# Optimization experiments

Hardware: AMD Instinct MI355X
Metric: run time of the kernel (lower is better)

Reference implementation:

```python
import jax, jax.numpy as jnp
import numpy as np
from jax import lax

B, S, M, D, H, T = 8, 128, 128, 256, 256, 256  # M == S required by reshape_adj; D == H required by tag FFNs and edge h0


def setup_inputs() -> dict:
    key = jax.random.key(0)
    ks = jax.random.split(key, 26)
    w = lambda k, shape: (jax.random.normal(k, shape, jnp.float32) * 0.05)
    lengths = jax.random.randint(ks[0], (B,), S // 2, S + 1)
    mask = (jnp.arange(S)[None, :] < lengths[:, None]).astype(jnp.int32)
    return {
        "input": jax.random.normal(ks[1], (B, S, D), jnp.float32),
        "tag_embeddings": jax.random.normal(ks[2], (B, S, 128), jnp.float32),
        "mask": mask,
        "head_indices": jax.random.randint(ks[3], (B, S), 0, S),
        "head_tags": jax.random.randint(ks[4], (B, S), 0, 40),
        # graph_rnn (2-layer tanh RNN, input D -> hidden H)
        "gW_ih0": w(ks[5], (H, D)), "gW_hh0": w(ks[6], (H, H)),
        "gb_ih0": w(ks[7], (H,)), "gb_hh0": w(ks[8], (H,)),
        "gW_ih1": w(ks[9], (H, H)), "gW_hh1": w(ks[10], (H, H)),
        "gb_ih1": w(ks[11], (H,)), "gb_hh1": w(ks[12], (H,)),
        # edge_rnn (2-layer tanh RNN, input M -> hidden H)
        "eW_ih0": w(ks[13], (H, M)), "eW_hh0": w(ks[14], (H, H)),
        "eb_ih0": w(ks[15], (H,)), "eb_hh0": w(ks[16], (H,)),
        "eW_ih1": w(ks[17], (H, H)), "eW_hh1": w(ks[18], (H, H)),
        "eb_ih1": w(ks[19], (H,)), "eb_hh1": w(ks[20], (H,)),
        # edge classifier + tag feedforwards
        "cls_W": w(ks[21], (1, H)), "cls_b": w(ks[22], (1,)),
        "head_W": w(ks[23], (T, H)), "head_b": jnp.zeros((T,), jnp.float32),
        "dep_W": w(ks[24], (T, H)), "dep_b": jnp.zeros((T,), jnp.float32),
    }


def _forward(input, gW_ih0, gW_hh0, gb_ih0, gb_hh0, gW_ih1, gW_hh1, gb_ih1, gb_hh1,
             eW_ih0, eW_hh0, eb_ih0, eb_hh0, eW_ih1, eW_hh1, eb_ih1, eb_hh1,
             cls_W, cls_b, head_W, head_b, dep_W, dep_b, mask):
    Bv, Sv, Dv = input.shape
    lengths = mask.sum(axis=-1)                      # [B]
    valid = jnp.arange(Sv)[:, None] < lengths[None, :]  # [S,B] packed-sequence validity

    # ---- graph_pass: 2-layer tanh RNN over time, emulating pack/pad (frozen state + zero output on pads)
    xt = input.transpose(1, 0, 2)  # [S,B,D]

    def gstep(h, inp):
        x_t, v = inp
        v = v[:, None]
        h0 = jnp.tanh(x_t @ gW_ih0.T + gb_ih0 + h[0] @ gW_hh0.T + gb_hh0)
        h0 = jnp.where(v, h0, h[0])
        h1 = jnp.tanh(h0 @ gW_ih1.T + gb_ih1 + h[1] @ gW_hh1.T + gb_hh1)
        h1 = jnp.where(v, h1, h[1])
        y = jnp.where(v, h1, 0.0)
        return jnp.stack([h0, h1]), y

    hg0 = jnp.zeros((2, Bv, H), input.dtype)
    _, ys = lax.scan(gstep, hg0, (xt, valid))
    graph_states = ys.transpose(1, 0, 2)  # [B,S,H]

    # ---- edge_pass: sequential over M steps; positions i are independent -> fold S into batch
    gs = graph_states.reshape(Bv * Sv, H)
    hE0 = jnp.stack([gs, gs])              # (edge_l=2, B*S, H)
    A0 = jnp.zeros((Bv * Sv, M), input.dtype)

    def estep(carry, j):
        A_row, h = carry
        x = A_row  # input at every step is the current (partially filled) row, per the original
        e0 = jnp.tanh(x @ eW_ih0.T + eb_ih0 + h[0] @ eW_hh0.T + eb_hh0)
        e1 = jnp.tanh(e0 @ eW_ih1.T + eb_ih1 + h[1] @ eW_hh1.T + eb_hh1)
        edge = jax.nn.sigmoid(e1 @ cls_W.T + cls_b)[:, 0]  # [B*S]
        A_row = A_row.at[:, j].set(edge)
        return (A_row, jnp.stack([e0, e1])), None

    (A_flat, _), _ = lax.scan(estep, (A0, hE0), jnp.arange(M))
    A = A_flat.reshape(Bv, Sv, M)

    # ---- reshape_adj: with M == S, shift is always 0 -> strictly-lower-triangular mask, then transpose
    tri = jnp.tril(jnp.ones((Sv, M), bool), -1)
    arc_logits = jnp.where(tri[None, :, :], A, 0.0).transpose(0, 2, 1)

    # ---- tag feedforwards (dropout = identity in eval mode)
    head_tag = jax.nn.elu(graph_states @ head_W.T + head_b)
    dep_tag = jax.nn.elu(graph_states @ dep_W.T + dep_b)
    return head_tag, dep_tag, arc_logits


def reference(input, tag_embeddings, mask, head_indices, head_tags,
              gW_ih0, gW_hh0, gb_ih0, gb_hh0, gW_ih1, gW_hh1, gb_ih1, gb_hh1,
              eW_ih0, eW_hh0, eb_ih0, eb_hh0, eW_ih1, eW_hh1, eb_ih1, eb_hh1,
              cls_W, cls_b, head_W, head_b, dep_W, dep_b):
    # tag_embeddings, head_indices, head_tags are passed through unchanged in the original
    return _forward(input, gW_ih0, gW_hh0, gb_ih0, gb_hh0, gW_ih1, gW_hh1, gb_ih1, gb_hh1,
                    eW_ih0, eW_hh0, eb_ih0, eb_hh0, eW_ih1, eW_hh1, eb_ih1, eb_hh1,
                    cls_W, cls_b, head_W, head_b, dep_W, dep_b, mask)
```

## Files before the change

kernel.cpp:

```cpp
#include <hip/hip_runtime.h>
#include <hip/hip_bf16.h>

#define HH 256
#define SS 128
#define BB 8
#define MM 128
#define DD 256
#define TT 256
#define GG 16
#define NW 8

#define ROWG 33
#define FBE (16 * ROWG * 8)
#define FB1 (ROWG * 8)

typedef float  f32x4  __attribute__((ext_vector_type(4)));
typedef short  bf16x8 __attribute__((ext_vector_type(8)));

__device__ __forceinline__ float bflo(unsigned int u) { return __uint_as_float(u << 16); }
__device__ __forceinline__ float bfhi(unsigned int u) { return __uint_as_float(u & 0xffff0000u); }
__device__ __forceinline__ float bfs(unsigned short s) { return __uint_as_float(((unsigned)s) << 16); }
__device__ __forceinline__ unsigned short f2bf(float x) {
    unsigned u = __float_as_uint(x);
    return (unsigned short)((u + 0x7fffu + ((u >> 16) & 1u)) >> 16);
}
__device__ __forceinline__ unsigned cvtpk(float lo, float hi) {
    unsigned r;
    asm("v_cvt_pk_bf16_f32 %0, %1, %2" : "=v"(r) : "v"(lo), "v"(hi));
    return r;
}
__device__ __forceinline__ float ftanh(float x) {
    float e = __expf(2.0f * x);
    return 1.0f - 2.0f * __builtin_amdgcn_rcpf(e + 1.0f);
}
__device__ __forceinline__ float fsigm(float x) {
    return __builtin_amdgcn_rcpf(1.0f + __expf(-x));
}

__global__ void k_prep(const float* __restrict__ gW_hh0, const float* __restrict__ gW_ih1,
                       const float* __restrict__ gW_hh1, const float* __restrict__ eW_hh0,
                       const float* __restrict__ eW_ih1, const float* __restrict__ eW_hh1,
                       const float* __restrict__ head_W, const float* __restrict__ dep_W,
                       const float* __restrict__ eW_ih0,
                       unsigned short* __restrict__ pk_g0, unsigned short* __restrict__ pk_g1,
                       unsigned short* __restrict__ pk_g2, unsigned short* __restrict__ pk_e0,
                       unsigned short* __restrict__ pk_e1, unsigned short* __restrict__ pk_e2,
                       unsigned short* __restrict__ pk_h0, unsigned short* __restrict__ pk_h1,
                       unsigned short* __restrict__ eWTb) {
    int m = blockIdx.x >> 5;
    int blk = blockIdx.x & 31;
    if (m < 8) {
        const float* W = (m == 0) ? gW_hh0 : (m == 1) ? gW_ih1 : (m == 2) ? gW_hh1
                       : (m == 3) ? eW_hh0 : (m == 4) ? eW_ih1 : (m == 5) ? eW_hh1
                       : (m == 6) ? head_W : dep_W;
        unsigned short* pk = (m == 0) ? pk_g0 : (m == 1) ? pk_g1 : (m == 2) ? pk_g2
                           : (m == 3) ? pk_e0 : (m == 4) ? pk_e1 : (m == 5) ? pk_e2
                           : (m == 6) ? pk_h0 : pk_h1;
        int idx = blk * 256 + threadIdx.x;
        int f = idx >> 6, l = idx & 63;
        int ct = f >> 3, kb = f & 7, q = l >> 4, mm = l & 15;
        unsigned short out[8];
#pragma unroll
        for (int e = 0; e < 8; e++) {
            int k = kb * 32 + q * 4 + (e & 3) + ((e >> 2) << 4);
            out[e] = f2bf(W[(ct * 16 + mm) * HH + k]);
        }
        uint4 v;
        v.x = out[0] | ((unsigned)out[1] << 16);
        v.y = out[2] | ((unsigned)out[3] << 16);
        v.z = out[4] | ((unsigned)out[5] << 16);
        v.w = out[6] | ((unsigned)out[7] << 16);
        *(uint4*)(pk + idx * 8) = v;
    } else {
        int base = blk * 256 + threadIdx.x;
#pragma unroll
        for (int k = 0; k < 4; k++) {
            int idx = base + k * 8192;
            int j = idx >> 8, c = idx & 255;
            eWTb[idx] = f2bf(eW_ih0[c * MM + j]);
        }
    }
}

__global__ void k_x0(const float* __restrict__ x, const float* __restrict__ Wih0,
                     const float* __restrict__ bih0, const float* __restrict__ bhh0,
                     unsigned short* __restrict__ X0B) {
    int row = blockIdx.x;
    int i = threadIdx.x;
    const float4* xr = (const float4*)(x + row * DD);
    const float4* wr = (const float4*)(Wih0 + i * DD);
    float a0 = 0.f, a1 = 0.f, a2 = 0.f, a3 = 0.f;
#pragma unroll 8
    for (int k = 0; k < DD / 4; k++) {
        float4 xv = xr[k]; float4 wv = wr[k];
        a0 += xv.x * wv.x; a1 += xv.y * wv.y; a2 += xv.z * wv.z; a3 += xv.w * wv.w;
    }
    X0B[row * HH + i] = f2bf(a0 + a1 + a2 + a3 + bih0[i] + bhh0[i]);
}

__device__ __forceinline__ bf16x8 ldA(const unsigned short* __restrict__ pk, int ct, int kb, int lane) {
    return *(const bf16x8*)(pk + (((ct * 8 + kb) * 64 + lane) << 3));
}
__device__ __forceinline__ bf16x8 ldBf(const unsigned short* base, int row, int kb, int q) {
    return *(const bf16x8*)(base + ((row * ROWG + kb * 4 + q) << 3));
}

__global__ __launch_bounds__(512, 2) void k_graph_mfma(
    const unsigned short* __restrict__ X0B, const int* __restrict__ mask,
    const unsigned short* __restrict__ pk0,
    const unsigned short* __restrict__ pk1,
    const unsigned short* __restrict__ pk2,
    const float* __restrict__ bih1, const float* __restrict__ bhh1,
    float* __restrict__ GS) {
    __shared__ alignas(16) unsigned short xs[SS * HH];
    __shared__ alignas(16) unsigned short gs[SS * HH];
    __shared__ alignas(16) unsigned short h0b[2 * FB1];
    __shared__ alignas(16) unsigned short h1b[3 * FB1];
    __shared__ int lenS;

    int b = blockIdx.x;
    int tid = threadIdx.x;
    int wv = tid >> 6, lane = tid & 63;
    int q = lane >> 4, rr = lane & 15;
    int ct0 = 2 * wv;
    int m0 = 32 * wv + 4 * q;
    int g16off = (wv * 4 + q) << 3;

    { unsigned* p = (unsigned*)h0b; for (int i = tid; i < FB1; i += 512) p[i] = 0; }
    { unsigned* p = (unsigned*)h1b; for (int i = tid; i < 3 * FB1 / 2; i += 512) p[i] = 0; }
    {
        const uint4* s = (const uint4*)(X0B + b * SS * HH);
        uint4* d = (uint4*)xs;
        for (int i = tid; i < SS * HH / 8; i += 512) d[i] = s[i];
    }
    if (wv == 0) {
        int s = mask[b * SS + lane] + mask[b * SS + 64 + lane];
        for (int off = 32; off; off >>= 1) s += __shfl_xor(s, off);
        if (lane == 0) lenS = s;
    }
    bf16x8 a0[2][8], a1[2][8], a2[2][8];
#pragma unroll
    for (int kb = 0; kb < 8; kb++) {
        a0[0][kb] = ldA(pk0, ct0, kb, lane); a0[1][kb] = ldA(pk0, ct0 + 1, kb, lane);
        a1[0][kb] = ldA(pk1, ct0, kb, lane); a1[1][kb] = ldA(pk1, ct0 + 1, kb, lane);
        a2[0][kb] = ldA(pk2, ct0, kb, lane); a2[1][kb] = ldA(pk2, ct0 + 1, kb, lane);
    }
#pragma unroll
    for (int kb = 0; kb < 8; kb++) {
        asm volatile("" : "+v"(a0[0][kb]), "+v"(a0[1][kb]),
                          "+v"(a1[0][kb]), "+v"(a1[1][kb]),
                          "+v"(a2[0][kb]), "+v"(a2[1][kb]));
    }
    f32x4 b1A = *(const f32x4*)(bih1 + m0) + *(const f32x4*)(bhh1 + m0);
    f32x4 b1B = *(const f32x4*)(bih1 + m0 + 16) + *(const f32x4*)(bhh1 + m0 + 16);
    __syncthreads();
    int len = lenS;
    bool w0l = (rr == 0);

    {
        ushort4 xa = *(const ushort4*)(xs + m0);
        ushort4 xb = *(const ushort4*)(xs + m0 + 16);
        if (w0l) {
            uint4 nv = { cvtpk(ftanh(bfs(xa.x)), ftanh(bfs(xa.y))),
                         cvtpk(ftanh(bfs(xa.z)), ftanh(bfs(xa.w))),
                         cvtpk(ftanh(bfs(xb.x)), ftanh(bfs(xb.y))),
                         cvtpk(ftanh(bfs(xb.z)), ftanh(bfs(xb.w))) };
            *(uint4*)(h0b + g16off) = nv;
        }
    }
    __syncthreads();

    ushort4 xcA = *(const ushort4*)(xs + 256 + m0);
    ushort4 xcB = *(const ushort4*)(xs + 256 + m0 + 16);

    int ir = 2, iw = 0;
    for (int t = 1; t < len; t++) {
        const unsigned short* h0r = h0b + ((t - 1) & 1) * FB1;
        const unsigned short* h1r = h1b + ir * FB1;
        int tn = (t + 1 < SS) ? t + 1 : t;
        ushort4 xnA = *(const ushort4*)(xs + tn * 256 + m0);
        ushort4 xnB = *(const ushort4*)(xs + tn * 256 + m0 + 16);
        f32x4 accA = { bfs(xcA.x), bfs(xcA.y), bfs(xcA.z), bfs(xcA.w) };
        f32x4 accB = { bfs(xcB.x), bfs(xcB.y), bfs(xcB.z), bfs(xcB.w) };
        f32x4 pAe = b1A, pBe = b1B;
        f32x4 pAh = {0.f,0.f,0.f,0.f}, pBh = {0.f,0.f,0.f,0.f};
#pragma unroll
        for (int kb = 0; kb < 8; kb++) {
            bf16x8 h = ldBf(h0r, 0, kb, q);
            bf16x8 g = ldBf(h1r, 0, kb, q);
            accA = __builtin_amdgcn_mfma_f32_16x16x32_bf16(a0[0][kb], h, accA, 0, 0, 0);
            accB = __builtin_amdgcn_mfma_f32_16x16x32_bf16(a0[1][kb], h, accB, 0, 0, 0);
            pAe  = __builtin_amdgcn_mfma_f32_16x16x32_bf16(a1[0][kb], h, pAe, 0, 0, 0);
            pBe  = __builtin_amdgcn_mfma_f32_16x16x32_bf16(a1[1][kb], h, pBe, 0, 0, 0);
            pAh  = __builtin_amdgcn_mfma_f32_16x16x32_bf16(a2[0][kb], g, pAh, 0, 0, 0);
            pBh  = __builtin_amdgcn_mfma_f32_16x16x32_bf16(a2[1][kb], g, pBh, 0, 0, 0);
        }
        if (w0l) {
            uint4 nv0 = { cvtpk(ftanh(accA[0]), ftanh(accA[1])), cvtpk(ftanh(accA[2]), ftanh(accA[3])),
                          cvtpk(ftanh(accB[0]), ftanh(accB[1])), cvtpk(ftanh(accB[2]), ftanh(accB[3])) };
            *(uint4*)(h0b + (t & 1) * FB1 + g16off) = nv0;
            f32x4 pA = pAe + pAh, pB = pBe + pBh;
            float eA[4], eB[4];
#pragma unroll
            for (int r = 0; r < 4; r++) { eA[r] = ftanh(pA[r]); eB[r] = ftanh(pB[r]); }
            uint4 nv1 = { cvtpk(eA[0], eA[1]), cvtpk(eA[2], eA[3]),
                          cvtpk(eB[0], eB[1]), cvtpk(eB[2], eB[3]) };
            *(uint4*)(h1b + iw * FB1 + g16off) = nv1;
            uint2 ga = { cvtpk(eA[0], eA[1]), cvtpk(eA[2], eA[3]) };
            uint2 gb = { cvtpk(eB[0], eB[1]), cvtpk(eB[2], eB[3]) };
            *(uint2*)(gs + (t - 1) * 256 + m0) = ga;
            *(uint2*)(gs + (t - 1) * 256 + m0 + 16) = gb;
        }
        __syncthreads();
        xcA = xnA; xcB = xnB;
        ir = (ir + 1 == 3) ? 0 : ir + 1;
        iw = (iw + 1 == 3) ? 0 : iw + 1;
    }

    {
        const unsigned short* h0r = h0b + ((len - 1) & 1) * FB1;
        const unsigned short* h1r = h1b + ir * FB1;
        f32x4 pAe = b1A, pBe = b1B;
        f32x4 pAh = {0.f,0.f,0.f,0.f}, pBh = {0.f,0.f,0.f,0.f};
#pragma unroll
        for (int kb = 0; kb < 8; kb++) {
            bf16x8 h = ldBf(h0r, 0, kb, q);
            bf16x8 g = ldBf(h1r, 0, kb, q);
            pAe = __builtin_amdgcn_mfma_f32_16x16x32_bf16(a1[0][kb], h, pAe, 0, 0, 0);
            pBe = __builtin_amdgcn_mfma_f32_16x16x32_bf16(a1[1][kb], h, pBe, 0, 0, 0);
            pAh = __builtin_amdgcn_mfma_f32_16x16x32_bf16(a2[0][kb], g, pAh, 0, 0, 0);
            pBh = __builtin_amdgcn_mfma_f32_16x16x32_bf16(a2[1][kb], g, pBh, 0, 0, 0);
        }
        if (w0l) {
            f32x4 pA = pAe + pAh, pB = pBe + pBh;
            uint2 ga = { cvtpk(ftanh(pA[0]), ftanh(pA[1])), cvtpk(ftanh(pA[2]), ftanh(pA[3])) };
            uint2 gb = { cvtpk(ftanh(pB[0]), ftanh(pB[1])), cvtpk(ftanh(pB[2]), ftanh(pB[3])) };
            *(uint2*)(gs + (len - 1) * 256 + m0) = ga;
            *(uint2*)(gs + (len - 1) * 256 + m0 + 16) = gb;
        }
    }
    __syncthreads();
    {
        float* dst = GS + b * (SS * HH);
        const uint4* src = (const uint4*)gs;
        for (int i = tid; i < SS * HH / 8; i += 512) {
            int t = i >> 5;
            float4 f0 = {0.f,0.f,0.f,0.f}, f1 = {0.f,0.f,0.f,0.f};
            if (t < len) {
                uint4 v = src[i];
                f0 = float4{ bflo(v.x), bfhi(v.x), bflo(v.y), bfhi(v.y) };
                f1 = float4{ bflo(v.z), bfhi(v.z), bflo(v.w), bfhi(v.w) };
            }
            *(float4*)(dst + i * 8) = f0;
            *(float4*)(dst + i * 8 + 4) = f1;
        }
    }
}

__global__ __launch_bounds__(512, 2) void k_edge_mfma(
    const float* __restrict__ GS,
    const unsigned short* __restrict__ pk0,
    const unsigned short* __restrict__ pk1,
    const unsigned short* __restrict__ pk2,
    const unsigned short* __restrict__ pkh,
    const unsigned short* __restrict__ pkd,
    const unsigned short* __restrict__ eWTb,
    const float* __restrict__ bih0, const float* __restrict__ bhh0,
    const float* __restrict__ bih1, const float* __restrict__ bhh1,
    const float* __restrict__ clsW, const float* __restrict__ clsB,
    const float* __restrict__ headB, const float* __restrict__ depB,
    float* __restrict__ arc, float* __restrict__ headO, float* __restrict__ depO) {
    __shared__ alignas(16) unsigned short h0[2 * FBE];
    __shared__ alignas(16) unsigned short h1[2 * FBE];
    __shared__ alignas(16) unsigned short gsf[FBE];
    __shared__ alignas(16) unsigned short ews[MM * HH];
    __shared__ float red[NW][GG];
    __shared__ float cws[HH];
    __shared__ float b1s[HH];
    __shared__ float arcb[GG][MM + 1];

    int tid = threadIdx.x;
    int wv = tid >> 6, lane = tid & 63;
    int q = lane >> 4, rr = lane & 15;
    int m0 = 32 * wv + 4 * q;
    int goff = (rr * ROWG + wv * 4 + q) << 3;
    int r0 = blockIdx.x * GG;

    {
        const uint4* s = (const uint4*)eWTb;
        uint4* d = (uint4*)ews;
        for (int i = tid; i < MM * HH / 8; i += 512) d[i] = s[i];
    }
    {
        int r = tid >> 5, g = tid & 31;
        int kb = g >> 2, qq = g & 3;
        int lo = kb * 32 + qq * 4;
        const float* gp = GS + (r0 + r) * HH + lo;
        float4 vlo = *(const float4*)gp;
        float4 vhi = *(const float4*)(gp + 16);
        uint4 pv = { cvtpk(vlo.x, vlo.y), cvtpk(vlo.z, vlo.w),
                     cvtpk(vhi.x, vhi.y), cvtpk(vhi.z, vhi.w) };
        int off = (r * ROWG + g) << 3;
        *(uint4*)(h0 + off) = pv;
        *(uint4*)(h1 + off) = pv;
        *(uint4*)(gsf + off) = pv;
    }
    if (tid < HH) {
        cws[tid] = clsW[tid];
        b1s[tid] = bih1[tid] + bhh1[tid];
    }
    bf16x8 a0[2][8], a1[2][8], a2[2][8];
#pragma unroll
    for (int kb = 0; kb < 8; kb++) {
        a0[0][kb] = ldA(pk0, 2 * wv, kb, lane); a0[1][kb] = ldA(pk0, 2 * wv + 1, kb, lane);
        a1[0][kb] = ldA(pk1, 2 * wv, kb, lane); a1[1][kb] = ldA(pk1, 2 * wv + 1, kb, lane);
        a2[0][kb] = ldA(pk2, 2 * wv, kb, lane); a2[1][kb] = ldA(pk2, 2 * wv + 1, kb, lane);
    }
#pragma unroll
    for (int kb = 0; kb < 8; kb++) {
        asm volatile("" : "+v"(a0[0][kb]), "+v"(a0[1][kb]),
                          "+v"(a1[0][kb]), "+v"(a1[1][kb]),
                          "+v"(a2[0][kb]), "+v"(a2[1][kb]));
    }
    f32x4 xw0A = *(const f32x4*)(bih0 + m0) + *(const f32x4*)(bhh0 + m0);
    f32x4 xw0B = *(const f32x4*)(bih0 + m0 + 16) + *(const f32x4*)(bhh0 + m0 + 16);
    float clsb = clsB[0];
    int srow = (r0 + tid) & 127;
    __syncthreads();

    ushort4 ewcA = *(const ushort4*)(ews + m0);
    ushort4 ewcB = *(const ushort4*)(ews + m0 + 16);

    for (int j = 0; j < MM; j++) {
        int jr = j & 1, jw = jr ^ 1;
        const unsigned short* rb0 = h0 + jr * FBE;
        f32x4 acc0 = xw0A, acc1 = xw0B;
#pragma unroll
        for (int kb = 0; kb < 8; kb++) {
            bf16x8 b = ldBf(rb0, rr, kb, q);
            acc0 = __builtin_amdgcn_mfma_f32_16x16x32_bf16(a0[0][kb], b, acc0, 0, 0, 0);
            acc1 = __builtin_amdgcn_mfma_f32_16x16x32_bf16(a0[1][kb], b, acc1, 0, 0, 0);
        }
        {
            uint4 nv = { cvtpk(ftanh(acc0[0]), ftanh(acc0[1])), cvtpk(ftanh(acc0[2]), ftanh(acc0[3])),
                         cvtpk(ftanh(acc1[0]), ftanh(acc1[1])), cvtpk(ftanh(acc1[2]), ftanh(acc1[3])) };
            *(uint4*)(h0 + jw * FBE + goff) = nv;
        }
        __syncthreads();
        int jn = (j + 1 < MM) ? j + 1 : j;
        ushort4 ewnA = *(const ushort4*)(ews + jn * HH + m0);
        ushort4 ewnB = *(const ushort4*)(ews + jn * HH + m0 + 16);
        const unsigned short* rn = h0 + jw * FBE;
        const unsigned short* r1 = h1 + jr * FBE;
        f32x4 p0e = *(const f32x4*)&b1s[m0];
        f32x4 p1e = *(const f32x4*)&b1s[m0 + 16];
        f32x4 p0h = {0.f,0.f,0.f,0.f}, p1h = {0.f,0.f,0.f,0.f};
#pragma unroll
        for (int kb = 0; kb < 8; kb++) {
            bf16x8 be = ldBf(rn, rr, kb, q);
            bf16x8 bh = ldBf(r1, rr, kb, q);
            p0e = __builtin_amdgcn_mfma_f32_16x16x32_bf16(a1[0][kb], be, p0e, 0, 0, 0);
            p1e = __builtin_amdgcn_mfma_f32_16x16x32_bf16(a1[1][kb], be, p1e, 0, 0, 0);
            p0h = __builtin_amdgcn_mfma_f32_16x16x32_bf16(a2[0][kb], bh, p0h, 0, 0, 0);
            p1h = __builtin_amdgcn_mfma_f32_16x16x32_bf16(a2[1][kb], bh, p1h, 0, 0, 0);
        }
        float e1a[4], e1b[4];
#pragma unroll
        for (int r = 0; r < 4; r++) { e1a[r] = ftanh(p0e[r] + p0h[r]); e1b[r] = ftanh(p1e[r] + p1h[r]); }
        {
            uint4 nv = { cvtpk(e1a[0], e1a[1]), cvtpk(e1a[2], e1a[3]),
                         cvtpk(e1b[0], e1b[1]), cvtpk(e1b[2], e1b[3]) };
            *(uint4*)(h1 + jw * FBE + goff) = nv;
        }
        f32x4 cwA = *(const f32x4*)&cws[m0];
        f32x4 cwB = *(const f32x4*)&cws[m0 + 16];
        float part = cwA[0] * e1a[0] + cwA[1] * e1a[1] + cwA[2] * e1a[2] + cwA[3] * e1a[3]
                   + cwB[0] * e1b[0] + cwB[1] * e1b[1] + cwB[2] * e1b[2] + cwB[3] * e1b[3];
        part += __shfl_xor(part, 16);
        part += __shfl_xor(part, 32);
        if (lane < 16) red[wv][lane] = part;
        __syncthreads();
        float s = clsb;
#pragma unroll
        for (int w = 0; w < NW; w++) s += red[w][rr];
        float edge = fsigm(s);
        f32x4 ewA = { bfs(ewcA.x), bfs(ewcA.y), bfs(ewcA.z), bfs(ewcA.w) };
        f32x4 ewB = { bfs(ewcB.x), bfs(ewcB.y), bfs(ewcB.z), bfs(ewcB.w) };
        xw0A += edge * ewA;
        xw0B += edge * ewB;
        if (tid < GG) arcb[tid][j] = (j < srow) ? edge : 0.f;
        ewcA = ewnA; ewcB = ewnB;
    }
    __syncthreads();
    for (int i = tid; i < GG * MM; i += 512) {
        int row = i & 15, j = i >> 4;
        int sr = (r0 + row) & 127, bi = (r0 + row) >> 7;
        arc[bi * (MM * SS) + j * SS + sr] = arcb[row][j];
    }
    {
        f32x4 hA = *(const f32x4*)(headB + m0);
        f32x4 hB = *(const f32x4*)(headB + m0 + 16);
        f32x4 dA = *(const f32x4*)(depB + m0);
        f32x4 dB = *(const f32x4*)(depB + m0 + 16);
#pragma unroll 1
        for (int kb = 0; kb < 8; kb++) {
            bf16x8 bg = ldBf(gsf, rr, kb, q);
            hA = __builtin_amdgcn_mfma_f32_16x16x32_bf16(ldA(pkh, 2 * wv, kb, lane), bg, hA, 0, 0, 0);
            hB = __builtin_amdgcn_mfma_f32_16x16x32_bf16(ldA(pkh, 2 * wv + 1, kb, lane), bg, hB, 0, 0, 0);
            dA = __builtin_amdgcn_mfma_f32_16x16x32_bf16(ldA(pkd, 2 * wv, kb, lane), bg, dA, 0, 0, 0);
            dB = __builtin_amdgcn_mfma_f32_16x16x32_bf16(ldA(pkd, 2 * wv + 1, kb, lane), bg, dB, 0, 0, 0);
        }
        int row = r0 + rr;
        f32x4 oA, oB, eA, eB;
#pragma unroll
        for (int r = 0; r < 4; r++) {
            oA[r] = (hA[r] > 0.f) ? hA[r] : (__expf(hA[r]) - 1.0f);
            oB[r] = (hB[r] > 0.f) ? hB[r] : (__expf(hB[r]) - 1.0f);
            eA[r] = (dA[r] > 0.f) ? dA[r] : (__expf(dA[r]) - 1.0f);
            eB[r] = (dB[r] > 0.f) ? dB[r] : (__expf(dB[r]) - 1.0f);
        }
        *(f32x4*)(headO + row * TT + m0) = oA;
        *(f32x4*)(headO + row * TT + m0 + 16) = oB;
        *(f32x4*)(depO + row * TT + m0) = eA;
        *(f32x4*)(depO + row * TT + m0 + 16) = eB;
    }
}

extern "C" void kernel_launch(void* const* d_in, const int* in_sizes, int n_in,
                              void* d_out, int out_size, void* d_ws, size_t ws_size,
                              hipStream_t stream) {
    const float* input  = (const float*)d_in[0];
    const int*   mask   = (const int*)d_in[2];
    const float* gW_ih0 = (const float*)d_in[5];
    const float* gW_hh0 = (const float*)d_in[6];
    const float* gb_ih0 = (const float*)d_in[7];
    const float* gb_hh0 = (const float*)d_in[8];
    const float* gW_ih1 = (const float*)d_in[9];
    const float* gW_hh1 = (const float*)d_in[10];
    const float* gb_ih1 = (const float*)d_in[11];
    const float* gb_hh1 = (const float*)d_in[12];
    const float* eW_ih0 = (const float*)d_in[13];
    const float* eW_hh0 = (const float*)d_in[14];
    const float* eb_ih0 = (const float*)d_in[15];
    const float* eb_hh0 = (const float*)d_in[16];
    const float* eW_ih1 = (const float*)d_in[17];
    const float* eW_hh1 = (const float*)d_in[18];
    const float* eb_ih1 = (const float*)d_in[19];
    const float* eb_hh1 = (const float*)d_in[20];
    const float* cls_W  = (const float*)d_in[21];
    const float* cls_b  = (const float*)d_in[22];
    const float* head_W = (const float*)d_in[23];
    const float* head_b = (const float*)d_in[24];
    const float* dep_W  = (const float*)d_in[25];
    const float* dep_b  = (const float*)d_in[26];

    float* out      = (float*)d_out;
    float* head_out = out;
    float* dep_out  = out + 262144;
    float* arc_out  = out + 524288;

    char* ws = (char*)d_ws;
    unsigned short* X0B = (unsigned short*)ws;
    float* GS  = (float*)(ws + (1 << 20));
    unsigned short* pk_g0 = (unsigned short*)(ws + (2 << 20));
    unsigned short* pk_g1 = pk_g0 + 65536;
    unsigned short* pk_g2 = pk_g0 + 2 * 65536;
    unsigned short* pk_e0 = pk_g0 + 3 * 65536;
    unsigned short* pk_e1 = pk_g0 + 4 * 65536;
    unsigned short* pk_e2 = pk_g0 + 5 * 65536;
    unsigned short* pk_h0 = pk_g0 + 6 * 65536;
    unsigned short* pk_h1 = pk_g0 + 7 * 65536;
    unsigned short* eWTb  = pk_g0 + 8 * 65536;

    k_prep<<<288, 256, 0, stream>>>(gW_hh0, gW_ih1, gW_hh1, eW_hh0, eW_ih1, eW_hh1,
                                    head_W, dep_W, eW_ih0,
                                    pk_g0, pk_g1, pk_g2, pk_e0, pk_e1, pk_e2,
                                    pk_h0, pk_h1, eWTb);
    k_x0<<<1024, 256, 0, stream>>>(input, gW_ih0, gb_ih0, gb_hh0, X0B);
    k_graph_mfma<<<8, 512, 0, stream>>>(X0B, mask, pk_g0, pk_g1, pk_g2, gb_ih1, gb_hh1, GS);
    k_edge_mfma<<<64, 512, 0, stream>>>(GS, pk_e0, pk_e1, pk_e2, pk_h0, pk_h1, eWTb,
                                        eb_ih0, eb_hh0, eb_ih1, eb_hh1, cls_W, cls_b,
                                        head_b, dep_b, arc_out, head_out, dep_out);
}
```

Baseline: 434.0 us.

## Software-pipeline edge RNN layers so layer-0 and layer-1 MFMAs share one pass

After: 430.8 us. No clear change (-0.7%).

```diff
diff --git a/kernel.cpp b/kernel.cpp
--- a/kernel.cpp
+++ b/kernel.cpp
@@ -270,8 +270,8 @@
     const float* __restrict__ clsW, const float* __restrict__ clsB,
     const float* __restrict__ headB, const float* __restrict__ depB,
     float* __restrict__ arc, float* __restrict__ headO, float* __restrict__ depO) {
-    __shared__ alignas(16) unsigned short h0[2 * FBE];
-    __shared__ alignas(16) unsigned short h1[2 * FBE];
+    __shared__ alignas(16) unsigned short h0f[2 * FBE];
+    __shared__ alignas(16) unsigned short h1f[2 * FBE];
     __shared__ alignas(16) unsigned short gsf[FBE];
     __shared__ alignas(16) unsigned short ews[MM * HH];
     __shared__ float red[NW][GG];
@@ -301,9 +301,11 @@
         uint4 pv = { cvtpk(vlo.x, vlo.y), cvtpk(vlo.z, vlo.w),
                      cvtpk(vhi.x, vhi.y), cvtpk(vhi.z, vhi.w) };
         int off = (r * ROWG + g) << 3;
-        *(uint4*)(h0 + off) = pv;
-        *(uint4*)(h1 + off) = pv;
+        *(uint4*)(h0f + FBE + off) = pv;
+        *(uint4*)(h1f + FBE + off) = pv;
         *(uint4*)(gsf + off) = pv;
+        *(uint4*)(h1f + off) = uint4{0,0,0,0};
+        *(uint4*)(h0f + off) = uint4{0,0,0,0};
     }
     if (tid < HH) {
         cws[tid] = clsW[tid];
@@ -328,70 +330,59 @@
     int srow = (r0 + tid) & 127;
     __syncthreads();
 
-    ushort4 ewcA = *(const ushort4*)(ews + m0);
-    ushort4 ewcB = *(const ushort4*)(ews + m0 + 16);
-
-    for (int j = 0; j < MM; j++) {
-        int jr = j & 1, jw = jr ^ 1;
-        const unsigned short* rb0 = h0 + jr * FBE;
+    for (int j = 0; j <= MM; j++) {
+        const unsigned short* h0r = h0f + ((j + 1) & 1) * FBE;
+        const unsigned short* h1r = h1f + (j & 1) * FBE;
         f32x4 acc0 = xw0A, acc1 = xw0B;
+        f32x4 p0 = *(const f32x4*)&b1s[m0];
+        f32x4 p1 = *(const f32x4*)&b1s[m0 + 16];
 #pragma unroll
         for (int kb = 0; kb < 8; kb++) {
-            bf16x8 b = ldBf(rb0, rr, kb, q);
-            acc0 = __builtin_amdgcn_mfma_f32_16x16x32_bf16(a0[0][kb], b, acc0, 0, 0, 0);
-            acc1 = __builtin_amdgcn_mfma_f32_16x16x32_bf16(a0[1][kb], b, acc1, 0, 0, 0);
-        }
-        {
+            bf16x8 b0 = ldBf(h0r, rr, kb, q);
+            bf16x8 b1 = ldBf(h1r, rr, kb, q);
+            acc0 = __builtin_amdgcn_mfma_f32_16x16x32_bf16(a0[0][kb], b0, acc0, 0, 0, 0);
+            acc1 = __builtin_amdgcn_mfma_f32_16x16x32_bf16(a0[1][kb], b0, acc1, 0, 0, 0);
+            p0   = __builtin_amdgcn_mfma_f32_16x16x32_bf16(a1[0][kb], b0, p0, 0, 0, 0);
+            p1   = __builtin_amdgcn_mfma_f32_16x16x32_bf16(a1[1][kb], b0, p1, 0, 0, 0);
+            p0   = __builtin_amdgcn_mfma_f32_16x16x32_bf16(a2[0][kb], b1, p0, 0, 0, 0);
+            p1   = __builtin_amdgcn_mfma_f32_16x16x32_bf16(a2[1][kb], b1, p1, 0, 0, 0);
+        }
+        if (j > 0) {
+            float e1a[4], e1b[4];
+#pragma unroll
+            for (int r = 0; r < 4; r++) { e1a[r] = ftanh(p0[r]); e1b[r] = ftanh(p1[r]); }
+            uint4 nv = { cvtpk(e1a[0], e1a[1]), cvtpk(e1a[2], e1a[3]),
+                         cvtpk(e1b[0], e1b[1]), cvtpk(e1b[2], e1b[3]) };
+            *(uint4*)(h1f + ((j + 1) & 1) * FBE + goff) = nv;
+            f32x4 cwA = *(const f32x4*)&cws[m0];
+            f32x4 cwB = *(const f32x4*)&cws[m0 + 16];
+            float part = cwA[0] * e1a[0] + cwA[1] * e1a[1] + cwA[2] * e1a[2] + cwA[3] * e1a[3]
+                       + cwB[0] * e1b[0] + cwB[1] * e1b[1] + cwB[2] * e1b[2] + cwB[3] * e1b[3];
+            part += __shfl_xor(part, 16);
+            part += __shfl_xor(part, 32);
+            if (lane < 16) red[wv][lane] = part;
+        }
+        __syncthreads();
+        if (j > 0) {
+            float s = clsb;
+#pragma unroll
+            for (int w = 0; w < NW; w++) s += red[w][rr];
+            float edge = fsigm(s);
+            ushort4 ewcA = *(const ushort4*)(ews + (j - 1) * HH + m0);
+            ushort4 ewcB = *(const ushort4*)(ews + (j - 1) * HH + m0 + 16);
+            f32x4 ewA = { bfs(ewcA.x), bfs(ewcA.y), bfs(ewcA.z), bfs(ewcA.w) };
+            f32x4 ewB = { bfs(ewcB.x), bfs(ewcB.y), bfs(ewcB.z), bfs(ewcB.w) };
+            xw0A += edge * ewA;  acc0 += edge * ewA;
+            xw0B += edge * ewB;  acc1 += edge * ewB;
+            if (tid < GG) arcb[tid][j - 1] = ((j - 1) < srow) ? edge : 0.f;
+        }
+        if (j < MM) {
             uint4 nv = { cvtpk(ftanh(acc0[0]), ftanh(acc0[1])), cvtpk(ftanh(acc0[2]), ftanh(acc0[3])),
                          cvtpk(ftanh(acc1[0]), ftanh(acc1[1])), cvtpk(ftanh(acc1[2]), ftanh(acc1[3])) };
-            *(uint4*)(h0 + jw * FBE + goff) = nv;
+            *(uint4*)(h0f + (j & 1) * FBE + goff) = nv;
         }
         __syncthreads();
-        int jn = (j + 1 < MM) ? j + 1 : j;
-        ushort4 ewnA = *(const ushort4*)(ews + jn * HH + m0);
-        ushort4 ewnB = *(const ushort4*)(ews + jn * HH + m0 + 16);
-        const unsigned short* rn = h0 + jw * FBE;
-        const unsigned short* r1 = h1 + jr * FBE;
-        f32x4 p0e = *(const f32x4*)&b1s[m0];
-        f32x4 p1e = *(const f32x4*)&b1s[m0 + 16];
-        f32x4 p0h = {0.f,0.f,0.f,0.f}, p1h = {0.f,0.f,0.f,0.f};
-#pragma unroll
-        for (int kb = 0; kb < 8; kb++) {
-            bf16x8 be = ldBf(rn, rr, kb, q);
-            bf16x8 bh = ldBf(r1, rr, kb, q);
-            p0e = __builtin_amdgcn_mfma_f32_16x16x32_bf16(a1[0][kb], be, p0e, 0, 0, 0);
-            p1e = __builtin_amdgcn_mfma_f32_16x16x32_bf16(a1[1][kb], be, p1e, 0, 0, 0);
-            p0h = __builtin_amdgcn_mfma_f32_16x16x32_bf16(a2[0][kb], bh, p0h, 0, 0, 0);
-            p1h = __builtin_amdgcn_mfma_f32_16x16x32_bf16(a2[1][kb], bh, p1h, 0, 0, 0);
-        }
-        float e1a[4], e1b[4];
-#pragma unroll
-        for (int r = 0; r < 4; r++) { e1a[r] = ftanh(p0e[r] + p0h[r]); e1b[r] = ftanh(p1e[r] + p1h[r]); }
-        {
-            uint4 nv = { cvtpk(e1a[0], e1a[1]), cvtpk(e1a[2], e1a[3]),
-                         cvtpk(e1b[0], e1b[1]), cvtpk(e1b[2], e1b[3]) };
-            *(uint4*)(h1 + jw * FBE + goff) = nv;
-        }
-        f32x4 cwA = *(const f32x4*)&cws[m0];
-        f32x4 cwB = *(const f32x4*)&cws[m0 + 16];
-        float part = cwA[0] * e1a[0] + cwA[1] * e1a[1] + cwA[2] * e1a[2] + cwA[3] * e1a[3]
-                   + cwB[0] * e1b[0] + cwB[1] * e1b[1] + cwB[2] * e1b[2] + cwB[3] * e1b[3];
-        part += __shfl_xor(part, 16);
-        part += __shfl_xor(part, 32);
-        if (lane < 16) red[wv][lane] = part;
-        __syncthreads();
-        float s = clsb;
-#pragma unroll
-        for (int w = 0; w < NW; w++) s += red[w][rr];
-        float edge = fsigm(s);
-        f32x4 ewA = { bfs(ewcA.x), bfs(ewcA.y), bfs(ewcA.z), bfs(ewcA.w) };
-        f32x4 ewB = { bfs(ewcB.x), bfs(ewcB.y), bfs(ewcB.z), bfs(ewcB.w) };
-        xw0A += edge * ewA;
-        xw0B += edge * ewB;
-        if (tid < GG) arcb[tid][j] = (j < srow) ? edge : 0.f;
-        ewcA = ewnA; ewcB = ewnB;
-    }
-    __syncthreads();
+    }
     for (int i = tid; i < GG * MM; i += 512) {
         int row = i & 15, j = i >> 4;
         int sr = (r0 + row) & 127, bi = (r0 + row) >> 7;
```
